# Optimization experiments

Hardware: AMD Instinct MI355X
Metric: run time of the kernel (lower is better)

Reference implementation:

```python
import jax, jax.numpy as jnp
import numpy as np

N_NODES = 100000
N_EDGES = 3200000
N_FEAT = 128
N_GRAPHS = 1024
N_CLASSES = 10
K = 30  # global_sort_pool k


def setup_inputs() -> dict:
    key = jax.random.key(0)
    ks = jax.random.split(key, 20)
    p = lambda k, shape: jax.random.normal(k, shape, jnp.float32) * 0.1
    return {
        "x": jax.random.normal(ks[0], (N_NODES, N_FEAT), jnp.float32),
        "w1": p(ks[1], (N_FEAT, 32)), "b1": p(ks[2], (32,)),
        "w2": p(ks[3], (32, 32)),     "b2": p(ks[4], (32,)),
        "w3": p(ks[5], (32, 32)),     "b3": p(ks[6], (32,)),
        "w4": p(ks[7], (32, 1)),      "b4": p(ks[8], (1,)),
        "conv5_w": p(ks[9], (16, 1, 97)),  "conv5_b": p(ks[10], (16,)),
        "conv6_w": p(ks[11], (32, 16, 5)), "conv6_b": p(ks[12], (32,)),
        "fc1_w": p(ks[13], (352, 128)),    "fc1_b": p(ks[14], (128,)),
        "fc2_w": p(ks[15], (128, N_CLASSES)), "fc2_b": p(ks[16], (N_CLASSES,)),
        "edge_src": jax.random.randint(ks[17], (N_EDGES,), 0, N_NODES),
        "edge_dst": jax.random.randint(ks[18], (N_EDGES,), 0, N_NODES),
        "batch": jnp.sort(jax.random.randint(ks[19], (N_NODES,), 0, N_GRAPHS)),
        "num_graphs": N_GRAPHS,
    }


def _gcn_forward(x, w1, b1, w2, b2, w3, b3, w4, b4,
                 conv5_w, conv5_b, conv6_w, conv6_b,
                 fc1_w, fc1_b, fc2_w, fc2_b,
                 edge_src, edge_dst, batch, num_graphs):
    n = x.shape[0]
    # remove_self_loops: mask self-loop edges to weight 0 (shapes stay static)
    ew = (edge_src != edge_dst).astype(x.dtype)
    # gcn_norm with added self-loops (weight 1): deg includes self-loop
    deg = jax.ops.segment_sum(ew, edge_dst, num_segments=n) + 1.0
    dis = jax.lax.rsqrt(deg)                       # deg^{-1/2}
    enorm = dis[edge_src] * dis[edge_dst] * ew     # [E]
    snorm = (dis * dis)[:, None]                   # self-loop norm [n,1]

    def gcn_conv(h, W, b):
        h = h @ W                                   # [n, out]
        agg = jax.ops.segment_sum(h[edge_src] * enorm[:, None], edge_dst,
                                  num_segments=n) + h * snorm
        return agg + b

    x1 = jnp.tanh(gcn_conv(x,  w1, b1))   # [n,32]
    x2 = jnp.tanh(gcn_conv(x1, w2, b2))   # [n,32]
    x3 = jnp.tanh(gcn_conv(x2, w3, b3))   # [n,32]
    x4 = jnp.tanh(gcn_conv(x3, w4, b4))   # [n,1]
    xc = jnp.concatenate([x1, x2, x3, x4], axis=-1)  # [n,97]

    # global_sort_pool(k=K): per-graph sort by last channel, descending
    key_last = xc[:, -1]
    order = jnp.lexsort((-key_last, batch))          # primary: batch, secondary: desc key
    bs = batch[order]                                # sorted graph ids
    counts = jax.ops.segment_sum(jnp.ones_like(batch, jnp.int32), batch,
                                 num_segments=num_graphs)
    starts = jnp.cumsum(counts) - counts             # exclusive prefix sum
    rank = jnp.arange(n) - starts[bs]                # rank within own graph
    r = jnp.where(rank < K, rank, K)                 # overflow -> dummy slot K
    pooled = jnp.zeros((num_graphs, K + 1, 97), xc.dtype)
    pooled = pooled.at[bs, r].set(xc[order])
    pooled = pooled[:, :K, :].reshape(num_graphs, 1, K * 97)  # [B,1,2910]

    # Conv1d(1,16,97,97) + relu
    h = jax.lax.conv_general_dilated(pooled, conv5_w, (97,), 'VALID',
                                     dimension_numbers=('NCH', 'OIH', 'NCH'))
    h = jax.nn.relu(h + conv5_b[None, :, None])      # [B,16,30]
    # MaxPool1d(2,2)
    h = jax.lax.reduce_window(h, -jnp.inf, jax.lax.max,
                              (1, 1, 2), (1, 1, 2), 'VALID')  # [B,16,15]
    # Conv1d(16,32,5,1) + relu
    h = jax.lax.conv_general_dilated(h, conv6_w, (1,), 'VALID',
                                     dimension_numbers=('NCH', 'OIH', 'NCH'))
    h = jax.nn.relu(h + conv6_b[None, :, None])      # [B,32,11]
    h = h.reshape(num_graphs, -1)                    # [B,352]

    h = jax.nn.relu(h @ fc1_w + fc1_b)               # [B,128]; dropout = identity (eval)
    return jax.nn.log_softmax(h @ fc2_w + fc2_b, axis=-1)  # [B,num_classes]


def reference(x, w1, b1, w2, b2, w3, b3, w4, b4,
              conv5_w, conv5_b, conv6_w, conv6_b,
              fc1_w, fc1_b, fc2_w, fc2_b,
              edge_src, edge_dst, batch, num_graphs):
    return _gcn_forward(x, w1, b1, w2, b2, w3, b3, w4, b4,
                        conv5_w, conv5_b, conv6_w, conv6_b,
                        fc1_w, fc1_b, fc2_w, fc2_b,
                        edge_src, edge_dst, batch, num_graphs)
```

## Files before the change

### kernel.cpp

```cpp
#include <hip/hip_runtime.h>
#include <hip/hip_bf16.h>

#define N_NODES 100000
#define N_EDGES 3200000
#define NGRAPH 1024
#define KTOP 30
#define PELEM (NGRAPH * KTOP * 97)

#define NBKT 782
#define NTILE 391
#define TILE 8192
#define BKT_CAP 4736

typedef __hip_bfloat16 bf16;
typedef float vfloat4 __attribute__((ext_vector_type(4)));

__device__ __forceinline__ float u2f(unsigned short h) {
    return __uint_as_float(((unsigned int)h) << 16);
}
__device__ __forceinline__ float LD(const void* p, int i, int bf) {
    if (bf) return u2f(((const unsigned short*)p)[i]);
    return ((const float*)p)[i];
}

__global__ void k_detect(const void* w1, int* flag) {
    if (threadIdx.x == 0 && blockIdx.x == 0) {
        const unsigned short* u = (const unsigned short*)w1;
        int plausible = 0;
        for (int i = 0; i < 64; i++) {
            float a = fabsf(u2f(u[2 * i]));
            if (a == 0.f || (a >= 9.765625e-4f && a <= 2.0f)) plausible++;
        }
        *flag = (plausible >= 40) ? 1 : 0;
    }
}

__global__ void k_icur(int* __restrict__ cur) {
    int i = blockIdx.x * 256 + threadIdx.x;
    if (i < NBKT) cur[i] = i * BKT_CAP;
}

__global__ __launch_bounds__(256) void k_scat(const int* __restrict__ src,
                                              const int* __restrict__ dst,
                                              int* __restrict__ cur,
                                              int* __restrict__ ebuf) {
    __shared__ int pk[TILE];
    __shared__ unsigned short bk[TILE];
    __shared__ int h[NBKT];
    __shared__ int base[NBKT];
    int tid = threadIdx.x;
    int ebase = blockIdx.x * TILE;
    for (int i = tid; i < NBKT; i += 256) h[i] = 0;
    __syncthreads();
    for (int i = tid; i < TILE; i += 256) {
        int e = ebase + i;
        int bkt = 0xFFFF;
        if (e < N_EDGES) {
            int s = __builtin_nontemporal_load(src + e);
            int d = __builtin_nontemporal_load(dst + e);
            if (s != d) {
                bkt = d >> 7;
                pk[i] = ((d & 127) << 17) | s;
                atomicAdd(&h[bkt], 1);
            }
        }
        bk[i] = (unsigned short)bkt;
    }
    __syncthreads();
    for (int i = tid; i < NBKT; i += 256) {
        int c = h[i];
        base[i] = c ? atomicAdd(&cur[i], c) : 0;
    }
    __syncthreads();
    for (int i = tid; i < NBKT; i += 256) h[i] = 0;
    __syncthreads();
    for (int i = tid; i < TILE; i += 256) {
        int bkt = bk[i];
        if (bkt != 0xFFFF) {
            int p = base[bkt] + atomicAdd(&h[bkt], 1);
            if (p < (bkt + 1) * BKT_CAP) ebuf[p] = pk[i];
        }
    }
}

__global__ __launch_bounds__(256) void k_bcnt(const int* __restrict__ ebuf,
                                              const int* __restrict__ cur,
                                              int* __restrict__ rs,
                                              int* __restrict__ re,
                                              float* __restrict__ dis,
                                              int* __restrict__ deg) {
    __shared__ int dloc[128];
    __shared__ int sc[128];
    int b = blockIdx.x;
    int node0 = b << 7;
    int nn = N_NODES - node0; if (nn > 128) nn = 128;
    int tid = threadIdx.x;
    if (tid < 128) dloc[tid] = 0;
    __syncthreads();
    int s = b * BKT_CAP;
    int cnt = cur[b] - s; if (cnt > BKT_CAP) cnt = BKT_CAP;
    int e = s + cnt;
    for (int i = s + tid; i < e; i += 256)
        atomicAdd(&dloc[ebuf[i] >> 17], 1);
    __syncthreads();
    if (tid < 128) sc[tid] = dloc[tid];
    __syncthreads();
    for (int off = 1; off < 128; off <<= 1) {
        int t = (tid >= off && tid < 128) ? sc[tid - off] : 0;
        __syncthreads();
        if (tid < 128) sc[tid] += t;
        __syncthreads();
    }
    if (tid < nn) {
        int st = s + sc[tid] - dloc[tid];
        rs[node0 + tid] = st;
        re[node0 + tid] = st + dloc[tid];
        dis[node0 + tid] = rsqrtf((float)dloc[tid] + 1.0f);
        deg[node0 + tid] = dloc[tid];
    }
}

__global__ __launch_bounds__(256) void k_bfill(const int* __restrict__ ebuf,
                                               const int* __restrict__ cur,
                                               const int* __restrict__ rs,
                                               const int* __restrict__ deg,
                                               int* __restrict__ csr) {
    __shared__ int cl[128];
    int b = blockIdx.x;
    int node0 = b << 7;
    int tid = threadIdx.x;
    if (tid < 128) {
        int n = node0 + tid;
        cl[tid] = (n < N_NODES) ? rs[n] : 0;
    }
    __syncthreads();
    int s = b * BKT_CAP;
    int cnt = cur[b] - s; if (cnt > BKT_CAP) cnt = BKT_CAP;
    int e = s + cnt;
    for (int i = s + tid; i < e; i += 256) {
        int pv = ebuf[i];
        int srcn = pv & 0x1FFFF;
        int pos = atomicAdd(&cl[pv >> 17], 1);
        int d = deg[srcn];
        csr[pos] = (d << 17) | srcn;
    }
}

__global__ void k_gstart(const int* __restrict__ batch, int* __restrict__ gstart) {
    int g = blockIdx.x * 256 + threadIdx.x;
    if (g > NGRAPH) return;
    int lo = 0, hi = N_NODES;
    while (lo < hi) {
        int mid = (lo + hi) >> 1;
        if (batch[mid] < g) lo = mid + 1; else hi = mid;
    }
    gstart[g] = lo;
}

#define MM1_B 64
__global__ __launch_bounds__(256) void k_mm1(const void* __restrict__ x,
                                             const void* __restrict__ w,
                                             const int* __restrict__ flagp,
                                             const float* __restrict__ dis,
                                             float* __restrict__ ts) {
    __shared__ float Xs[MM1_B][129];
    __shared__ float Wf[128 * 32];
    int bf = *flagp;
    int tid = threadIdx.x;
    int nbase = blockIdx.x * MM1_B;
    if (bf) {
        const ushort4* wv = (const ushort4*)w;
        for (int idx = tid; idx < 1024; idx += 256) {
            ushort4 h = wv[idx];
            int p = idx * 4;
            Wf[p] = u2f(h.x); Wf[p + 1] = u2f(h.y); Wf[p + 2] = u2f(h.z); Wf[p + 3] = u2f(h.w);
        }
        const unsigned short* xb = (const unsigned short*)x;
        for (int idx = tid; idx < 1024; idx += 256) {
            int row = idx >> 4, c8 = (idx & 15) * 8;
            int gn = nbase + row; if (gn >= N_NODES) gn = N_NODES - 1;
            uint4 v = *(const uint4*)(xb + (size_t)gn * 128 + c8);
            float* d = &Xs[row][c8];
            d[0] = u2f((unsigned short)(v.x & 0xffff)); d[1] = u2f((unsigned short)(v.x >> 16));
            d[2] = u2f((unsigned short)(v.y & 0xffff)); d[3] = u2f((unsigned short)(v.y >> 16));
            d[4] = u2f((unsigned short)(v.z & 0xffff)); d[5] = u2f((unsigned short)(v.z >> 16));
            d[6] = u2f((unsigned short)(v.w & 0xffff)); d[7] = u2f((unsigned short)(v.w >> 16));
        }
    } else {
        const float* wf = (const float*)w;
        for (int idx = tid; idx < 4096; idx += 256) Wf[idx] = wf[idx];
        const float4* xv = (const float4*)x;
        for (int idx = tid; idx < 2048; idx += 256) {
            int row = idx >> 5, c4 = (idx & 31) * 4;
            int gn = nbase + row; if (gn >= N_NODES) gn = N_NODES - 1;
            float4 v = xv[(size_t)gn * 32 + (c4 >> 2)];
            float* d = &Xs[row][c4];
            d[0] = v.x; d[1] = v.y; d[2] = v.z; d[3] = v.w;
        }
    }
    __syncthreads();
    int tn = (tid & 15) * 4;
    int tc = (tid >> 4) * 2;
    float a00 = 0.f, a01 = 0.f, a10 = 0.f, a11 = 0.f;
    float a20 = 0.f, a21 = 0.f, a30 = 0.f, a31 = 0.f;
#pragma unroll 4
    for (int k = 0; k < 128; k++) {
        float2 wv = *(const float2*)&Wf[k * 32 + tc];
        float x0 = Xs[tn + 0][k], x1 = Xs[tn + 1][k];
        float x2 = Xs[tn + 2][k], x3 = Xs[tn + 3][k];
        a00 += x0 * wv.x; a01 += x0 * wv.y;
        a10 += x1 * wv.x; a11 += x1 * wv.y;
        a20 += x2 * wv.x; a21 += x2 * wv.y;
        a30 += x3 * wv.x; a31 += x3 * wv.y;
    }
    int n0 = nbase + tn;
    if (n0 + 0 < N_NODES) { float d = dis[n0 + 0]; *(float2*)&ts[(n0 + 0) * 32 + tc] = make_float2(d * a00, d * a01); }
    if (n0 + 1 < N_NODES) { float d = dis[n0 + 1]; *(float2*)&ts[(n0 + 1) * 32 + tc] = make_float2(d * a10, d * a11); }
    if (n0 + 2 < N_NODES) { float d = dis[n0 + 2]; *(float2*)&ts[(n0 + 2) * 32 + tc] = make_float2(d * a20, d * a21); }
    if (n0 + 3 < N_NODES) { float d = dis[n0 + 3]; *(float2*)&ts[(n0 + 3) * 32 + tc] = make_float2(d * a30, d * a31); }
}

__global__ __launch_bounds__(256) void k_agg(const float4* __restrict__ ts,
                                             const int* __restrict__ rs,
                                             const int* __restrict__ re,
                                             const int* __restrict__ csr,
                                             const float* __restrict__ dis,
                                             const void* __restrict__ b,
                                             const int* __restrict__ flagp,
                                             float4* __restrict__ out) {
    int node = blockIdx.x * 4 + (threadIdx.x >> 6);
    int lane = threadIdx.x & 63;
    int q   = lane & 7;
    int grp = lane >> 3;
    int bf = *flagp;
    int s = rs[node], e = re[node];
    float4 a0 = make_float4(0.f, 0.f, 0.f, 0.f);
    float4 a1 = a0, a2 = a0, a3 = a0;
    int i = s + grp;
    for (; i + 24 < e; i += 32) {
        int v0 = csr[i] & 0x1FFFF, v1 = csr[i + 8] & 0x1FFFF;
        int v2 = csr[i + 16] & 0x1FFFF, v3 = csr[i + 24] & 0x1FFFF;
        float4 m0 = ts[v0 * 8 + q];
        float4 m1 = ts[v1 * 8 + q];
        float4 m2 = ts[v2 * 8 + q];
        float4 m3 = ts[v3 * 8 + q];
        a0.x += m0.x; a0.y += m0.y; a0.z += m0.z; a0.w += m0.w;
        a1.x += m1.x; a1.y += m1.y; a1.z += m1.z; a1.w += m1.w;
        a2.x += m2.x; a2.y += m2.y; a2.z += m2.z; a2.w += m2.w;
        a3.x += m3.x; a3.y += m3.y; a3.z += m3.z; a3.w += m3.w;
    }
    for (; i < e; i += 8) {
        float4 m = ts[(csr[i] & 0x1FFFF) * 8 + q];
        a0.x += m.x; a0.y += m.y; a0.z += m.z; a0.w += m.w;
    }
    float4 acc;
    acc.x = (a0.x + a1.x) + (a2.x + a3.x);
    acc.y = (a0.y + a1.y) + (a2.y + a3.y);
    acc.z = (a0.z + a1.z) + (a2.z + a3.z);
    acc.w = (a0.w + a1.w) + (a2.w + a3.w);
#pragma unroll
    for (int off = 8; off < 64; off <<= 1) {
        acc.x += __shfl_xor(acc.x, off);
        acc.y += __shfl_xor(acc.y, off);
        acc.z += __shfl_xor(acc.z, off);
        acc.w += __shfl_xor(acc.w, off);
    }
    if (grp == 0) {
        float4 self = ts[node * 8 + q];
        float d = dis[node];
        vfloat4 r;
        r.x = tanhf(d * (acc.x + self.x) + LD(b, q * 4 + 0, bf));
        r.y = tanhf(d * (acc.y + self.y) + LD(b, q * 4 + 1, bf));
        r.z = tanhf(d * (acc.z + self.z) + LD(b, q * 4 + 2, bf));
        r.w = tanhf(d * (acc.w + self.w) + LD(b, q * 4 + 3, bf));
        __builtin_nontemporal_store(r, (vfloat4*)&out[node * 8 + q]);
    }
}

template<int DO_TS4>
__global__ __launch_bounds__(256) void k_aggz(const float4* __restrict__ xin,
                                              const int* __restrict__ rs,
                                              const int* __restrict__ re,
                                              const int* __restrict__ csr,
                                              const float* __restrict__ dis,
                                              const void* __restrict__ W,
                                              const void* __restrict__ b,
                                              const void* __restrict__ w4,
                                              const int* __restrict__ flagp,
                                              float* __restrict__ xout,
                                              float* __restrict__ ts4) {
    __shared__ float Wl[1024];
    __shared__ float W4l[32];
    __shared__ float Z[4][32];
    int tid = threadIdx.x;
    int bf = *flagp;
    if (bf) {
        ushort4 h = ((const ushort4*)W)[tid];
        int p = tid * 4;
        Wl[p] = u2f(h.x); Wl[p + 1] = u2f(h.y); Wl[p + 2] = u2f(h.z); Wl[p + 3] = u2f(h.w);
    } else {
        float4 v = ((const float4*)W)[tid];
        int p = tid * 4;
        Wl[p] = v.x; Wl[p + 1] = v.y; Wl[p + 2] = v.z; Wl[p + 3] = v.w;
    }
    if (DO_TS4 && tid < 32) W4l[tid] = LD(w4, tid, bf);

    int wid = tid >> 6;
    int node = blockIdx.x * 4 + wid;
    int lane = tid & 63;
    int q   = lane & 7;
    int grp = lane >> 3;
    int s = rs[node], e = re[node];
    float4 a0 = make_float4(0.f, 0.f, 0.f, 0.f);
    float4 a1 = a0, a2 = a0, a3 = a0;
    int i = s + grp;
    for (; i + 24 < e; i += 32) {
        int p0 = csr[i], p1 = csr[i + 8], p2 = csr[i + 16], p3 = csr[i + 24];
        int v0 = p0 & 0x1FFFF, v1 = p1 & 0x1FFFF, v2 = p2 & 0x1FFFF, v3 = p3 & 0x1FFFF;
        float d0 = rsqrtf((float)(p0 >> 17) + 1.0f);
        float d1 = rsqrtf((float)(p1 >> 17) + 1.0f);
        float d2 = rsqrtf((float)(p2 >> 17) + 1.0f);
        float d3 = rsqrtf((float)(p3 >> 17) + 1.0f);
        float4 m0 = xin[v0 * 8 + q];
        float4 m1 = xin[v1 * 8 + q];
        float4 m2 = xin[v2 * 8 + q];
        float4 m3 = xin[v3 * 8 + q];
        a0.x += d0 * m0.x; a0.y += d0 * m0.y; a0.z += d0 * m0.z; a0.w += d0 * m0.w;
        a1.x += d1 * m1.x; a1.y += d1 * m1.y; a1.z += d1 * m1.z; a1.w += d1 * m1.w;
        a2.x += d2 * m2.x; a2.y += d2 * m2.y; a2.z += d2 * m2.z; a2.w += d2 * m2.w;
        a3.x += d3 * m3.x; a3.y += d3 * m3.y; a3.z += d3 * m3.z; a3.w += d3 * m3.w;
    }
    for (; i < e; i += 8) {
        int pv = csr[i];
        int v = pv & 0x1FFFF;
        float dv = rsqrtf((float)(pv >> 17) + 1.0f);
        float4 m = xin[v * 8 + q];
        a0.x += dv * m.x; a0.y += dv * m.y; a0.z += dv * m.z; a0.w += dv * m.w;
    }
    float4 acc;
    acc.x = (a0.x + a1.x) + (a2.x + a3.x);
    acc.y = (a0.y + a1.y) + (a2.y + a3.y);
    acc.z = (a0.z + a1.z) + (a2.z + a3.z);
    acc.w = (a0.w + a1.w) + (a2.w + a3.w);
#pragma unroll
    for (int off = 8; off < 64; off <<= 1) {
        acc.x += __shfl_xor(acc.x, off);
        acc.y += __shfl_xor(acc.y, off);
        acc.z += __shfl_xor(acc.z, off);
        acc.w += __shfl_xor(acc.w, off);
    }
    if (grp == 0) {
        float4 self = xin[node * 8 + q];
        float di = dis[node];
        Z[wid][q * 4 + 0] = acc.x + di * self.x;
        Z[wid][q * 4 + 1] = acc.y + di * self.y;
        Z[wid][q * 4 + 2] = acc.z + di * self.z;
        Z[wid][q * 4 + 3] = acc.w + di * self.w;
    }
    __syncthreads();
    int nd = tid >> 6;
    int col = tid & 31;
    int kbase = (tid & 32) >> 1;
    const float* zr = Z[nd];
    float a = 0.f;
#pragma unroll
    for (int k2 = 0; k2 < 16; k2++) a += zr[kbase + k2] * Wl[(kbase + k2) * 32 + col];
    a += __shfl_xor(a, 32);
    int n2 = blockIdx.x * 4 + nd;
    float di2 = dis[n2];
    float xo = tanhf(di2 * a + LD(b, col, bf));
    if (!(tid & 32)) xout[n2 * 32 + col] = xo;
    if (DO_TS4) {
        float t4 = xo * W4l[col];
#pragma unroll
        for (int off = 1; off < 32; off <<= 1) t4 += __shfl_xor(t4, off);
        if ((tid & 63) == 0) ts4[n2] = di2 * t4;
    }
}

__global__ __launch_bounds__(256) void k_agg1(const float* __restrict__ ts4,
                                              const int* __restrict__ rs,
                                              const int* __restrict__ re,
                                              const int* __restrict__ csr,
                                              const float* __restrict__ dis,
                                              const void* __restrict__ b4,
                                              const int* __restrict__ flagp,
                                              float* __restrict__ x4) {
    int node = blockIdx.x * 16 + (threadIdx.x >> 4);
    int lane = threadIdx.x & 15;
    int s = rs[node], e = re[node];
    float acc = 0.f;
    for (int i = s + lane; i < e; i += 16) acc += ts4[csr[i] & 0x1FFFF];
#pragma unroll
    for (int off = 1; off < 16; off <<= 1) acc += __shfl_xor(acc, off);
    if (lane == 0) {
        int bf = *flagp;
        x4[node] = tanhf(dis[node] * (acc + ts4[node]) + LD(b4, 0, bf));
    }
}

__global__ __launch_bounds__(256) void k_rank(const int* __restrict__ batch,
                                              const int* __restrict__ gstart,
                                              const float* __restrict__ x4,
                                              int* __restrict__ sel) {
    int i = blockIdx.x * 256 + threadIdx.x;
    if (i >= N_NODES) return;
    int g = batch[i];
    int s = gstart[g], e = gstart[g + 1];
    float ki = x4[i];
    int rank = 0;
    for (int j = s; j < e; j++) {
        float kj = x4[j];
        rank += (kj > ki) || (kj == ki && j < i);
    }
    if (rank < KTOP) sel[g * KTOP + rank] = i;
}

__global__ __launch_bounds__(256) void k_pool(const float* __restrict__ x1,
                                              const float* __restrict__ x2,
                                              const float* __restrict__ x3,
                                              const float* __restrict__ x4,
                                              const int* __restrict__ sel,
                                              float* __restrict__ P) {
    int idx = blockIdx.x * 256 + threadIdx.x;
    if (idx >= PELEM) return;
    int g = idx / (KTOP * 97);
    int r = idx - g * (KTOP * 97);
    int p = r / 97;
    int f = r - p * 97;
    int v = sel[g * KTOP + p];
    float val = 0.f;
    if (v >= 0) {
        if (f < 32)      val = x1[v * 32 + f];
        else if (f < 64) val = x2[v * 32 + f - 32];
        else if (f < 96) val = x3[v * 32 + f - 64];
        else             val = x4[v];
    }
    P[idx] = val;
}

__global__ __launch_bounds__(256) void k_head(
    const float* __restrict__ Pg,
    const void* __restrict__ w5, const void* __restrict__ b5,
    const void* __restrict__ w6, const void* __restrict__ b6,
    const void* __restrict__ f1w, const void* __restrict__ f1b,
    const void* __restrict__ f2w, const void* __restrict__ f2b,
    const int* __restrict__ flagp, void* __restrict__ out) {
    __shared__ float P[KTOP * 97];
    __shared__ float W5[16 * 97];
    __shared__ float W6[32 * 16 * 5];
    __shared__ float H5[16][30];
    __shared__ float M[16][15];
    __shared__ float H6[352];
    __shared__ float Rp[256];
    __shared__ float R1[128];
    __shared__ float L[10];
    __shared__ float mls;
    int g = blockIdx.x;
    int tid = threadIdx.x;
    int bf = *flagp;

    for (int i = tid; i < KTOP * 97; i += 256) P[i] = Pg[g * (KTOP * 97) + i];
    if (bf) {
        const ushort4* w5v = (const ushort4*)w5;
        for (int i = tid; i < 388; i += 256) {
            ushort4 h = w5v[i];
            int p = i * 4;
            W5[p] = u2f(h.x); W5[p + 1] = u2f(h.y); W5[p + 2] = u2f(h.z); W5[p + 3] = u2f(h.w);
        }
        const ushort4* w6v = (const ushort4*)w6;
        for (int i = tid; i < 640; i += 256) {
            ushort4 h = w6v[i];
            int p = i * 4;
            W6[p] = u2f(h.x); W6[p + 1] = u2f(h.y); W6[p + 2] = u2f(h.z); W6[p + 3] = u2f(h.w);
        }
    } else {
        for (int i = tid; i < 16 * 97; i += 256) W5[i] = ((const float*)w5)[i];
        for (int i = tid; i < 2560; i += 256) W6[i] = ((const float*)w6)[i];
    }
    __syncthreads();
    for (int idx = tid; idx < 480; idx += 256) {
        int o = idx / 30, p = idx - o * 30;
        float acc = LD(b5, o, bf);
        const float* pr = &P[p * 97];
        const float* wr = &W5[o * 97];
        for (int f = 0; f < 97; f++) acc += wr[f] * pr[f];
        H5[o][p] = fmaxf(acc, 0.f);
    }
    __syncthreads();
    for (int idx = tid; idx < 240; idx += 256) {
        int o = idx / 15, q = idx - o * 15;
        M[o][q] = fmaxf(H5[o][2 * q], H5[o][2 * q + 1]);
    }
    __syncthreads();
    for (int idx = tid; idx < 352; idx += 256) {
        int oc = idx / 11, tp = idx - oc * 11;
        float acc = LD(b6, oc, bf);
        const float* wr = &W6[oc * 80];
        for (int ic = 0; ic < 16; ic++) {
#pragma unroll
            for (int k = 0; k < 5; k++)
                acc += wr[ic * 5 + k] * M[ic][tp + k];
        }
        H6[idx] = fmaxf(acc, 0.f);
    }
    __syncthreads();
    {
        int half = tid >> 7, col = tid & 127;
        int base = half * 176;
        float a = 0.f;
        for (int i = 0; i < 176; i++) {
            int ii = base + i;
            a += H6[ii] * LD(f1w, ii * 128 + col, bf);
        }
        Rp[tid] = a;
    }
    __syncthreads();
    if (tid < 128) R1[tid] = fmaxf(LD(f1b, tid, bf) + Rp[tid] + Rp[128 + tid], 0.f);
    __syncthreads();
    if (tid < 10) {
        float acc = LD(f2b, tid, bf);
        for (int k = 0; k < 128; k++) acc += R1[k] * LD(f2w, k * 10 + tid, bf);
        L[tid] = acc;
    }
    __syncthreads();
    if (tid == 0) {
        float m = L[0];
        for (int c = 1; c < 10; c++) m = fmaxf(m, L[c]);
        float ssum = 0.f;
        for (int c = 0; c < 10; c++) ssum += expf(L[c] - m);
        mls = m + logf(ssum);
    }
    __syncthreads();
    if (tid < 10) {
        float v = L[tid] - mls;
        if (bf) ((bf16*)out)[g * 10 + tid] = __float2bfloat16(v);
        else    ((float*)out)[g * 10 + tid] = v;
    }
}

extern "C" void kernel_launch(void* const* d_in, const int* in_sizes, int n_in,
                              void* d_out, int out_size, void* d_ws, size_t ws_size,
                              hipStream_t stream) {
    const void* x   = d_in[0];
    const void* w1  = d_in[1];  const void* b1  = d_in[2];
    const void* w2  = d_in[3];  const void* b2  = d_in[4];
    const void* w3  = d_in[5];  const void* b3  = d_in[6];
    const void* w4  = d_in[7];  const void* b4  = d_in[8];
    const void* w5  = d_in[9];  const void* b5  = d_in[10];
    const void* w6  = d_in[11]; const void* b6  = d_in[12];
    const void* f1w = d_in[13]; const void* f1b = d_in[14];
    const void* f2w = d_in[15]; const void* f2b = d_in[16];
    const int* esrc  = (const int*)d_in[17];
    const int* edst  = (const int*)d_in[18];
    const int* batch = (const int*)d_in[19];

    char* w = (char*)d_ws;
    size_t off = 0;
    auto alloc = [&](size_t bytes) {
        void* p = w + off;
        off += (bytes + 255) & ~(size_t)255;
        return p;
    };
    int*   flag   = (int*)  alloc(256);
    int*   rs     = (int*)  alloc((size_t)N_NODES * 4);
    int*   re     = (int*)  alloc((size_t)N_NODES * 4);
    float* dis    = (float*)alloc((size_t)N_NODES * 4);
    int*   deg    = (int*)  alloc((size_t)N_NODES * 4);
    int*   csr    = (int*)  alloc((size_t)NBKT * BKT_CAP * 4);
    float* t      = (float*)alloc((size_t)N_NODES * 32 * 4);
    float* x1     = (float*)alloc((size_t)N_NODES * 32 * 4);
    float* x2     = (float*)alloc((size_t)N_NODES * 32 * 4);
    float* x3     = (float*)alloc((size_t)N_NODES * 32 * 4);
    float* x4     = (float*)alloc((size_t)N_NODES * 4);
    float* ts4b   = (float*)alloc((size_t)N_NODES * 4);
    int*   gstart = (int*)  alloc((size_t)(NGRAPH + 1) * 4);
    int*   sel    = (int*)  alloc((size_t)NGRAPH * KTOP * 4);
    float* Pg     = (float*)alloc((size_t)PELEM * 4);
    int*   cur    = (int*)  alloc((size_t)NBKT * 4);
    (void)ws_size; (void)n_in; (void)in_sizes; (void)out_size;

    int* ebuf = (int*)t;

    (void)hipMemsetAsync(sel, 0xFF, (size_t)NGRAPH * KTOP * 4, stream);

    int nb   = (N_NODES + 255) / 256;
    int mb64 = (N_NODES + MM1_B - 1) / MM1_B;
    int ab   = N_NODES / 4;
    int a1b  = N_NODES / 16;
    int pb   = (PELEM + 255) / 256;

    k_detect<<<1, 64, 0, stream>>>(w1, flag);
    k_icur<<<(NBKT + 255) / 256, 256, 0, stream>>>(cur);
    k_scat<<<NTILE, 256, 0, stream>>>(esrc, edst, cur, ebuf);
    k_bcnt<<<NBKT, 256, 0, stream>>>(ebuf, cur, rs, re, dis, deg);
    k_bfill<<<NBKT, 256, 0, stream>>>(ebuf, cur, rs, deg, csr);
    k_gstart<<<5, 256, 0, stream>>>(batch, gstart);

    k_mm1<<<mb64, 256, 0, stream>>>(x, w1, flag, dis, t);
    k_agg<<<ab, 256, 0, stream>>>((const float4*)t, rs, re, csr, dis, b1, flag, (float4*)x1);
    k_aggz<0><<<ab, 256, 0, stream>>>((const float4*)x1, rs, re, csr, dis, w2, b2, w4, flag, x2, ts4b);
    k_aggz<1><<<ab, 256, 0, stream>>>((const float4*)x2, rs, re, csr, dis, w3, b3, w4, flag, x3, ts4b);
    k_agg1<<<a1b, 256, 0, stream>>>(ts4b, rs, re, csr, dis, b4, flag, x4);
    k_rank<<<nb, 256, 0, stream>>>(batch, gstart, x4, sel);
    k_pool<<<pb, 256, 0, stream>>>(x1, x2, x3, x4, sel, Pg);
    k_head<<<NGRAPH, 256, 0, stream>>>(Pg, w5, b5, w6, b6,
                                       f1w, f1b, f2w, f2b, flag, (void*)d_out);
}
```

Measured before the change: 561.3 us.

## Fuse top-k ranking and pooling gather into the per-graph head kernel

Replaces the separate rank, pool and memset steps with per-graph work inside k_head. Each block loads its graph's x4 keys into shared memory, ranks the nodes there, gathers the selected rows directly into shared P, then runs the conv with padded rows and float4 dot products. This drops two launches, a memset and the global P buffer round trip. The cost is that ranking now runs on only 1024 blocks, so large graphs get less parallelism, and graphs above 512 nodes fall back to global reads.

```diff
diff --git a/kernel.cpp b/kernel.cpp
--- a/kernel.cpp
+++ b/kernel.cpp
@@ -5,12 +5,12 @@
 #define N_EDGES 3200000
 #define NGRAPH 1024
 #define KTOP 30
-#define PELEM (NGRAPH * KTOP * 97)
 
 #define NBKT 782
 #define NTILE 391
 #define TILE 8192
 #define BKT_CAP 4736
+#define GMAX 512
 
 typedef __hip_bfloat16 bf16;
 typedef float vfloat4 __attribute__((ext_vector_type(4)));
@@ -399,75 +399,41 @@
     }
 }
 
-__global__ __launch_bounds__(256) void k_rank(const int* __restrict__ batch,
-                                              const int* __restrict__ gstart,
-                                              const float* __restrict__ x4,
-                                              int* __restrict__ sel) {
-    int i = blockIdx.x * 256 + threadIdx.x;
-    if (i >= N_NODES) return;
-    int g = batch[i];
-    int s = gstart[g], e = gstart[g + 1];
-    float ki = x4[i];
-    int rank = 0;
-    for (int j = s; j < e; j++) {
-        float kj = x4[j];
-        rank += (kj > ki) || (kj == ki && j < i);
-    }
-    if (rank < KTOP) sel[g * KTOP + rank] = i;
-}
-
-__global__ __launch_bounds__(256) void k_pool(const float* __restrict__ x1,
-                                              const float* __restrict__ x2,
-                                              const float* __restrict__ x3,
-                                              const float* __restrict__ x4,
-                                              const int* __restrict__ sel,
-                                              float* __restrict__ P) {
-    int idx = blockIdx.x * 256 + threadIdx.x;
-    if (idx >= PELEM) return;
-    int g = idx / (KTOP * 97);
-    int r = idx - g * (KTOP * 97);
-    int p = r / 97;
-    int f = r - p * 97;
-    int v = sel[g * KTOP + p];
-    float val = 0.f;
-    if (v >= 0) {
-        if (f < 32)      val = x1[v * 32 + f];
-        else if (f < 64) val = x2[v * 32 + f - 32];
-        else if (f < 96) val = x3[v * 32 + f - 64];
-        else             val = x4[v];
-    }
-    P[idx] = val;
-}
-
 __global__ __launch_bounds__(256) void k_head(
-    const float* __restrict__ Pg,
+    const float* __restrict__ x1, const float* __restrict__ x2,
+    const float* __restrict__ x3, const float* __restrict__ x4,
+    const int* __restrict__ gstart,
     const void* __restrict__ w5, const void* __restrict__ b5,
     const void* __restrict__ w6, const void* __restrict__ b6,
     const void* __restrict__ f1w, const void* __restrict__ f1b,
     const void* __restrict__ f2w, const void* __restrict__ f2b,
     const int* __restrict__ flagp, void* __restrict__ out) {
-    __shared__ float P[KTOP * 97];
-    __shared__ float W5[16 * 97];
+    __shared__ float P[KTOP * 100];
+    __shared__ float W5[16 * 100];
     __shared__ float W6[32 * 16 * 5];
     __shared__ float H5[16][30];
     __shared__ float M[16][15];
     __shared__ float H6[352];
     __shared__ float Rp[256];
     __shared__ float R1[128];
+    __shared__ float keys[GMAX];
+    __shared__ int   selL[KTOP];
     __shared__ float L[10];
     __shared__ float mls;
     int g = blockIdx.x;
     int tid = threadIdx.x;
     int bf = *flagp;
-
-    for (int i = tid; i < KTOP * 97; i += 256) P[i] = Pg[g * (KTOP * 97) + i];
+    int s = gstart[g], e = gstart[g + 1];
+    int gsize = e - s;
+    int gl = gsize < GMAX ? gsize : GMAX;
+
+    if (tid < KTOP) selL[tid] = -1;
+    for (int i = tid; i < gl; i += 256) keys[i] = x4[s + i];
+    for (int i = tid; i < 16 * 97; i += 256) {
+        int o = i / 97, f = i - o * 97;
+        W5[o * 100 + f] = LD(w5, i, bf);
+    }
     if (bf) {
-        const ushort4* w5v = (const ushort4*)w5;
-        for (int i = tid; i < 388; i += 256) {
-            ushort4 h = w5v[i];
-            int p = i * 4;
-            W5[p] = u2f(h.x); W5[p + 1] = u2f(h.y); W5[p + 2] = u2f(h.z); W5[p + 3] = u2f(h.w);
-        }
         const ushort4* w6v = (const ushort4*)w6;
         for (int i = tid; i < 640; i += 256) {
             ushort4 h = w6v[i];
@@ -475,16 +441,48 @@
             W6[p] = u2f(h.x); W6[p + 1] = u2f(h.y); W6[p + 2] = u2f(h.z); W6[p + 3] = u2f(h.w);
         }
     } else {
-        for (int i = tid; i < 16 * 97; i += 256) W5[i] = ((const float*)w5)[i];
         for (int i = tid; i < 2560; i += 256) W6[i] = ((const float*)w6)[i];
+    }
+    __syncthreads();
+    for (int li = tid; li < gsize; li += 256) {
+        float ki = (li < GMAX) ? keys[li] : x4[s + li];
+        int rank = 0;
+        for (int j = 0; j < gl; j++) {
+            float kj = keys[j];
+            rank += (kj > ki) || (kj == ki && j < li);
+        }
+        for (int j = GMAX; j < gsize; j++) {
+            float kj = x4[s + j];
+            rank += (kj > ki) || (kj == ki && j < li);
+        }
+        if (rank < KTOP) selL[rank] = s + li;
+    }
+    __syncthreads();
+    for (int idx = tid; idx < KTOP * 97; idx += 256) {
+        int p = idx / 97, f = idx - p * 97;
+        int v = selL[p];
+        float val = 0.f;
+        if (v >= 0) {
+            if (f < 32)      val = x1[v * 32 + f];
+            else if (f < 64) val = x2[v * 32 + f - 32];
+            else if (f < 96) val = x3[v * 32 + f - 64];
+            else             val = x4[v];
+        }
+        P[p * 100 + f] = val;
     }
     __syncthreads();
     for (int idx = tid; idx < 480; idx += 256) {
         int o = idx / 30, p = idx - o * 30;
         float acc = LD(b5, o, bf);
-        const float* pr = &P[p * 97];
-        const float* wr = &W5[o * 97];
-        for (int f = 0; f < 97; f++) acc += wr[f] * pr[f];
+        const float* pr = &P[p * 100];
+        const float* wr = &W5[o * 100];
+#pragma unroll 6
+        for (int f4 = 0; f4 < 24; f4++) {
+            float4 a = *(const float4*)(pr + f4 * 4);
+            float4 b = *(const float4*)(wr + f4 * 4);
+            acc += b.x * a.x; acc += b.y * a.y; acc += b.z * a.z; acc += b.w * a.w;
+        }
+        acc += wr[96] * pr[96];
         H5[o][p] = fmaxf(acc, 0.f);
     }
     __syncthreads();
@@ -575,20 +573,14 @@
     float* x4     = (float*)alloc((size_t)N_NODES * 4);
     float* ts4b   = (float*)alloc((size_t)N_NODES * 4);
     int*   gstart = (int*)  alloc((size_t)(NGRAPH + 1) * 4);
-    int*   sel    = (int*)  alloc((size_t)NGRAPH * KTOP * 4);
-    float* Pg     = (float*)alloc((size_t)PELEM * 4);
     int*   cur    = (int*)  alloc((size_t)NBKT * 4);
     (void)ws_size; (void)n_in; (void)in_sizes; (void)out_size;
 
     int* ebuf = (int*)t;
 
-    (void)hipMemsetAsync(sel, 0xFF, (size_t)NGRAPH * KTOP * 4, stream);
-
-    int nb   = (N_NODES + 255) / 256;
     int mb64 = (N_NODES + MM1_B - 1) / MM1_B;
     int ab   = N_NODES / 4;
     int a1b  = N_NODES / 16;
-    int pb   = (PELEM + 255) / 256;
 
     k_detect<<<1, 64, 0, stream>>>(w1, flag);
     k_icur<<<(NBKT + 255) / 256, 256, 0, stream>>>(cur);
@@ -602,8 +594,7 @@
     k_aggz<0><<<ab, 256, 0, stream>>>((const float4*)x1, rs, re, csr, dis, w2, b2, w4, flag, x2, ts4b);
     k_aggz<1><<<ab, 256, 0, stream>>>((const float4*)x2, rs, re, csr, dis, w3, b3, w4, flag, x3, ts4b);
     k_agg1<<<a1b, 256, 0, stream>>>(ts4b, rs, re, csr, dis, b4, flag, x4);
-    k_rank<<<nb, 256, 0, stream>>>(batch, gstart, x4, sel);
-    k_pool<<<pb, 256, 0, stream>>>(x1, x2, x3, x4, sel, Pg);
-    k_head<<<NGRAPH, 256, 0, stream>>>(Pg, w5, b5, w6, b6,
+    k_head<<<NGRAPH, 256, 0, stream>>>(x1, x2, x3, x4, gstart,
+                                       w5, b5, w6, b6,
                                        f1w, f1b, f2w, f2b, flag, (void*)d_out);
 }
```

Result: faster. 538.4 us (-4.1%).
